# Performance work log

Measured on AMD Instinct MI355X. Metric: run time of the kernel, lower is better.

The kernel has to match this reference:

```python
import jax, jax.numpy as jnp
import numpy as np

DEPTH, DIM, HEADS, DH = 2, 1024, 16, 64
B, N, MEM, TEXT = 8, 256, 4, 64
PH, PW, PS = 4, 4, 16
EXP_H, EXP_W, EXP_T = 4, 4, 2
RH, RW, RT = 2*EXP_H+1, 2*EXP_W+1, 2*EXP_T+1  # 9,9,5
CUR_IDX = 20
MEM_IDXS = [0, 5, 10, 15]
SCALE = DH ** -0.5


def _pos(idx):
    # get_pos_from_idx_down_right
    nf = PH * PW
    inner = idx % nf
    return inner % PH, inner // PH, idx // nf


def _axial_freqs():
    # 2D axial rotary freqs over the (PH*PS)x(PW*PS) pixel grid, rot_dim = DH
    GH, GW = PH * PS, PW * PS
    nfa = DH // 4  # 16 base freqs per axis -> 32 dims per axis after pair-repeat
    inv = 1.0 / (10000.0 ** (np.arange(nfa, dtype=np.float64) / nfa))
    fh = np.repeat(np.arange(GH)[:, None] * inv[None, :], 2, axis=-1)  # [GH,32]
    fw = np.repeat(np.arange(GW)[:, None] * inv[None, :], 2, axis=-1)  # [GW,32]
    return np.concatenate([
        np.broadcast_to(fh[:, None, :], (GH, GW, DH // 2)),
        np.broadcast_to(fw[None, :, :], (GH, GW, DH // 2)),
    ], axis=-1).astype(np.float32)  # [GH,GW,DH]


def setup_inputs() -> dict:
    key = jax.random.key(0)
    ks = jax.random.split(key, 14)
    p = lambda k, shape: jax.random.normal(k, shape, jnp.float32) * 0.02
    x = jax.random.normal(ks[0], (B, N, DIM), jnp.float32)
    cond = jax.random.normal(ks[1], (B, MEM * N + TEXT, DIM), jnp.float32)
    Wq = p(ks[2], (DEPTH, DIM, HEADS * DH))
    Wk = p(ks[3], (DEPTH, DIM, HEADS * DH))
    Wv = p(ks[4], (DEPTH, DIM, HEADS * DH))
    Wo = p(ks[5], (DEPTH, HEADS * DH, DIM))
    bo = jnp.zeros((DEPTH, DIM), jnp.float32)
    rpe = p(ks[6], (DEPTH, RH * RW * RT, HEADS))
    W1 = p(ks[7], (DEPTH, DIM, DIM * 4 * 2))
    b1 = jnp.zeros((DEPTH, DIM * 8), jnp.float32)
    W2 = p(ks[8], (DEPTH, DIM * 4, DIM))
    b2 = jnp.zeros((DEPTH, DIM), jnp.float32)
    freqs = _axial_freqs()
    def block(idx):
        r, c, _ = _pos(idx)
        return freqs[r * PS:(r + 1) * PS, c * PS:(c + 1) * PS].reshape(-1, DH)
    src_freq = jnp.asarray(block(CUR_IDX))
    tgt_freq = jnp.asarray(np.concatenate([block(i) for i in MEM_IDXS], axis=0))
    sr, sc, st = _pos(CUR_IDX)
    rel = [(tr - sr + EXP_H) * RW + (tc - sc + EXP_W) + (tt - st + EXP_T) * RH * RW
           for (tr, tc, tt) in map(_pos, MEM_IDXS)]
    rel_idx = jnp.asarray(rel, jnp.int32)
    return dict(x=x, cond=cond, Wq=Wq, Wk=Wk, Wv=Wv, Wo=Wo, bo=bo, rpe=rpe,
                W1=W1, b1=b1, W2=W2, b2=b2, src_freq=src_freq, tgt_freq=tgt_freq,
                rel_idx=rel_idx)


def _rotate_half(t):
    # pairs interleaved: (d r) with r=2
    tr = t.reshape(t.shape[:-1] + (-1, 2))
    t1, t2 = tr[..., 0], tr[..., 1]
    return jnp.stack((-t2, t1), axis=-1).reshape(t.shape)


def _apply_rotary(freqs, t):
    return t * jnp.cos(freqs) + _rotate_half(t) * jnp.sin(freqs)


def reference(x, cond, Wq, Wk, Wv, Wo, bo, rpe, W1, b1, W2, b2, src_freq, tgt_freq, rel_idx):
    MS = MEM * N  # memory token count in cond
    split_heads = lambda t: t.reshape(t.shape[0], t.shape[1], HEADS, DH).transpose(0, 2, 1, 3)
    for l in range(DEPTH):
        # --- FullCrossAttention ---
        q = split_heads(x @ Wq[l])          # [b,h,n,dh]
        k = split_heads(cond @ Wk[l])       # [b,h,j,dh]
        v = split_heads(cond @ Wv[l])
        # gathered relative-position bias added to k (broadcast over feature dim)
        bias = rpe[l][rel_idx]              # [mem, h]
        bias_k = jnp.repeat(bias.T, N, axis=1)[None, :, :, None]  # [1,h,mem*S,1]
        k = k.at[:, :, :MS, :].add(bias_k)
        # inline rotary: src freqs on q, gathered target freqs on memory keys
        q = _apply_rotary(src_freq, q)
        k = k.at[:, :, :MS, :].set(_apply_rotary(tgt_freq, k[:, :, :MS, :]))
        dots = jnp.einsum('bhid,bhjd->bhij', q, k) * SCALE
        attn = jax.nn.softmax(dots, axis=-1)
        out = jnp.einsum('bhij,bhjd->bhid', attn, v)
        out = out.transpose(0, 2, 1, 3).reshape(x.shape[0], N, HEADS * DH)
        x = x + out @ Wo[l] + bo[l]
        # --- GEGLU FeedForward ---
        hgl = x @ W1[l] + b1[l]
        a, g = jnp.split(hgl, 2, axis=-1)
        y = a * jax.nn.gelu(g, approximate=False)
        x = x + y @ W2[l] + b2[l]
    return x
```

## Files before the change

kernel.cpp:

```cpp
#include <hip/hip_runtime.h>
#include <hip/hip_bf16.h>
#include <math.h>

typedef __hip_bfloat16 bf16;
typedef __bf16 bf16x8 __attribute__((ext_vector_type(8)));
typedef float f32x4 __attribute__((ext_vector_type(4)));

typedef __attribute__((address_space(3))) void lds_void;
typedef const __attribute__((address_space(1))) void gbl_void;

__device__ __forceinline__ float b2f(bf16 v) { return __bfloat162float(v); }
__device__ __forceinline__ bf16 f2b(float v) { return __float2bfloat16(v); }

__device__ __forceinline__ f32x4 shfl_xor4(f32x4 v, int m) {
  f32x4 o;
  o[0] = __shfl_xor(v[0], m);
  o[1] = __shfl_xor(v[1], m);
  o[2] = __shfl_xor(v[2], m);
  o[3] = __shfl_xor(v[3], m);
  return o;
}
__device__ __forceinline__ f32x4 max4(f32x4 a, f32x4 b) {
  f32x4 o;
  o[0] = fmaxf(a[0], b[0]); o[1] = fmaxf(a[1], b[1]);
  o[2] = fmaxf(a[2], b[2]); o[3] = fmaxf(a[3], b[3]);
  return o;
}
__device__ __forceinline__ f32x4 exp4(f32x4 a) {
  f32x4 o;
  o[0] = __expf(a[0]); o[1] = __expf(a[1]);
  o[2] = __expf(a[2]); o[3] = __expf(a[3]);
  return o;
}

__device__ __forceinline__ void cbar(int ahead) {
  if (ahead >= 2)      asm volatile("s_waitcnt vmcnt(8)" ::: "memory");
  else if (ahead == 1) asm volatile("s_waitcnt vmcnt(4)" ::: "memory");
  else                 asm volatile("s_waitcnt vmcnt(0)" ::: "memory");
  __builtin_amdgcn_s_barrier();
  __builtin_amdgcn_sched_barrier(0);
}

__global__ void detect_dtype(const unsigned int* __restrict__ x, int* __restrict__ flag) {
  int cnt = 0;
  for (int i = 0; i < 128; ++i) {
    unsigned int lo = x[i] & 0xFFFFu;
    unsigned int e = (lo >> 7) & 0xFFu;
    if (e >= 100u && e <= 140u) ++cnt;
  }
  *flag = (cnt >= 96) ? 1 : 0;
}

__global__ void convert_in(const void* __restrict__ src, bf16* __restrict__ dst,
                           int n, const int* __restrict__ flag) {
  int i = blockIdx.x * 256 + threadIdx.x;
  if (i >= n) return;
  dst[i] = (*flag) ? ((const bf16*)src)[i] : f2b(((const float*)src)[i]);
}

__global__ void emit_kernel(const float* __restrict__ xf, const int* __restrict__ flag,
                            void* __restrict__ out) {
  int i = blockIdx.x * 256 + threadIdx.x;
  if (*flag) ((bf16*)out)[i] = f2b(xf[i]);
  else       ((float*)out)[i] = xf[i];
}

template<int HALF>
__device__ __forceinline__ bf16x8 frag_ld(const __bf16* lt, int r, int quad) {
  constexpr int LB = (HALF == 128) ? 7 : 6;
  int line = r & (HALF - 1);
  int sl = (((r >> LB) << 2) | quad) ^ (line & 7);
  return *(const bf16x8*)&lt[line * 64 + sl * 8];
}

template<int TAG>
__global__ __launch_bounds__(256, 2) void gemm_bt(
    const bf16* __restrict__ A, int lda,
    const bf16* __restrict__ Bt, int ldb,
    float alpha,
    const float* __restrict__ resid,
    const bf16* __restrict__ bias,
    float* __restrict__ outf,
    bf16* __restrict__ outb,
    int ldc, int K)
{
  __shared__ char smem[65536] __attribute__((aligned(16)));
  float* lC = (float*)smem;

  int tid = threadIdx.x;
  int lane = tid & 63;
  int wave = tid >> 6;
  int quad = lane >> 4, l16 = lane & 15;
  int wm = (wave >> 1) * 64, wn = (wave & 1) * 64;
  int row0 = blockIdx.y * 128, col0 = blockIdx.x * 128;

  const bf16* asrc[2]; const bf16* bsrc[2];
#pragma unroll
  for (int i = 0; i < 2; ++i) {
    int line = i * 32 + (tid >> 3);
    int hx = (tid & 7) ^ (line & 7);
    int r = line + ((hx >> 2) << 6);
    int ke = (hx & 3) << 3;
    asrc[i] = A + (long long)(row0 + r) * lda + ke;
    bsrc[i] = Bt + (long long)(col0 + r) * ldb + ke;
  }

  auto stage = [&](int b, int t) {
    int o = t * 32;
#pragma unroll
    for (int i = 0; i < 2; ++i) {
      __builtin_amdgcn_global_load_lds((gbl_void*)(asrc[i] + o),
          (lds_void*)(smem + b * 8192 + i * 4096 + wave * 1024), 16, 0, 0);
      __builtin_amdgcn_global_load_lds((gbl_void*)(bsrc[i] + o),
          (lds_void*)(smem + 32768 + b * 8192 + i * 4096 + wave * 1024), 16, 0, 0);
    }
  };

  f32x4 acc[4][4];
#pragma unroll
  for (int a = 0; a < 4; ++a)
#pragma unroll
    for (int b = 0; b < 4; ++b) acc[a][b] = (f32x4){0.f, 0.f, 0.f, 0.f};

  int nk = K >> 5;
  stage(0, 0); stage(1, 1); stage(2, 2);
  cbar(2);

  for (int t = 0; t < nk; ++t) {
    if (t + 3 < nk) stage((t + 3) & 3, t + 3);
    const __bf16* lA = (const __bf16*)(smem + (t & 3) * 8192);
    const __bf16* lB = (const __bf16*)(smem + 32768 + (t & 3) * 8192);
    bf16x8 af[4], bfr[4];
#pragma unroll
    for (int mi = 0; mi < 4; ++mi) af[mi] = frag_ld<64>(lA, wm + mi * 16 + l16, quad);
#pragma unroll
    for (int ni = 0; ni < 4; ++ni) bfr[ni] = frag_ld<64>(lB, wn + ni * 16 + l16, quad);
    __builtin_amdgcn_s_setprio(1);
#pragma unroll
    for (int mi = 0; mi < 4; ++mi)
#pragma unroll
      for (int ni = 0; ni < 4; ++ni)
        acc[mi][ni] = __builtin_amdgcn_mfma_f32_16x16x32_bf16(
            af[mi], bfr[ni], acc[mi][ni], 0, 0, 0);
    __builtin_amdgcn_s_setprio(0);
    int hi = t + 3; if (hi > nk - 1) hi = nk - 1;
    cbar(hi - (t + 1));
  }

#pragma unroll
  for (int half = 0; half < 2; ++half) {
    __syncthreads();
    if ((wave >> 1) == half) {
#pragma unroll
      for (int mi = 0; mi < 4; ++mi)
#pragma unroll
        for (int ni = 0; ni < 4; ++ni)
#pragma unroll
          for (int r = 0; r < 4; ++r)
            lC[(mi * 16 + quad * 4 + r) * 128 + wn + ni * 16 + l16] =
                acc[mi][ni][r] * alpha;
    }
    __syncthreads();
#pragma unroll
    for (int i = 0; i < 8; ++i) {
      int f = i * 256 + tid;
      int row = f >> 5, cc = (f & 31) * 4;
      int m = row0 + half * 64 + row, n = col0 + cc;
      f32x4 v = *(const f32x4*)&lC[row * 128 + cc];
      long long ci = (long long)m * ldc + n;
      if (bias) {
        v[0] += b2f(bias[n]);     v[1] += b2f(bias[n + 1]);
        v[2] += b2f(bias[n + 2]); v[3] += b2f(bias[n + 3]);
      }
      if (resid) v += *(const f32x4*)&resid[ci];
      if (outf) *(f32x4*)&outf[ci] = v;
      if (outb) {
        bf16 c0 = f2b(v[0]), c1 = f2b(v[1]), c2 = f2b(v[2]), c3 = f2b(v[3]);
        ushort4 o = { *(unsigned short*)&c0, *(unsigned short*)&c1,
                      *(unsigned short*)&c2, *(unsigned short*)&c3 };
        *(ushort4*)&outb[ci] = o;
      }
    }
  }
}

__global__ __launch_bounds__(512, 2) void gemm256(
    const bf16* __restrict__ A, int lda,
    const bf16* __restrict__ Bt, int ldb,
    const bf16* __restrict__ bias,
    bf16* __restrict__ outb,
    int ldc, int K)
{
  __shared__ char smem[131072] __attribute__((aligned(16)));
  float* lC = (float*)smem;

  int tid = threadIdx.x;
  int lane = tid & 63;
  int wave = tid >> 6;
  int quad = lane >> 4, l16 = lane & 15;
  int wr = wave >> 2, wc = wave & 3;
  int wm = wr * 128, wn = wc * 64;
  int row0 = blockIdx.y * 256, col0 = blockIdx.x * 256;

  const bf16* asrc[2]; const bf16* bsrc[2];
#pragma unroll
  for (int i = 0; i < 2; ++i) {
    int line = i * 64 + (tid >> 3);
    int hx = (tid & 7) ^ (line & 7);
    int r = line + ((hx >> 2) << 7);
    int ke = (hx & 3) << 3;
    asrc[i] = A + (long long)(row0 + r) * lda + ke;
    bsrc[i] = Bt + (long long)(col0 + r) * ldb + ke;
  }

  auto stage = [&](int b, int t) {
    int o = t * 32;
#pragma unroll
    for (int i = 0; i < 2; ++i) {
      __builtin_amdgcn_global_load_lds((gbl_void*)(asrc[i] + o),
          (lds_void*)(smem + b * 16384 + i * 8192 + wave * 1024), 16, 0, 0);
      __builtin_amdgcn_global_load_lds((gbl_void*)(bsrc[i] + o),
          (lds_void*)(smem + 65536 + b * 16384 + i * 8192 + wave * 1024), 16, 0, 0);
    }
  };

  f32x4 acc[8][4];
#pragma unroll
  for (int a = 0; a < 8; ++a)
#pragma unroll
    for (int b = 0; b < 4; ++b) acc[a][b] = (f32x4){0.f, 0.f, 0.f, 0.f};

  int nk = K >> 5;
  stage(0, 0); stage(1, 1); stage(2, 2);
  cbar(2);

  for (int t = 0; t < nk; ++t) {
    if (t + 3 < nk) stage((t + 3) & 3, t + 3);
    const __bf16* lA = (const __bf16*)(smem + (t & 3) * 16384);
    const __bf16* lB = (const __bf16*)(smem + 65536 + (t & 3) * 16384);
    bf16x8 af[8], bfr[4];
#pragma unroll
    for (int mi = 0; mi < 8; ++mi) af[mi] = frag_ld<128>(lA, wm + mi * 16 + l16, quad);
#pragma unroll
    for (int ni = 0; ni < 4; ++ni) bfr[ni] = frag_ld<128>(lB, wn + ni * 16 + l16, quad);
    __builtin_amdgcn_s_setprio(1);
#pragma unroll
    for (int mi = 0; mi < 8; ++mi)
#pragma unroll
      for (int ni = 0; ni < 4; ++ni)
        acc[mi][ni] = __builtin_amdgcn_mfma_f32_16x16x32_bf16(
            af[mi], bfr[ni], acc[mi][ni], 0, 0, 0);
    __builtin_amdgcn_s_setprio(0);
    int hi = t + 3; if (hi > nk - 1) hi = nk - 1;
    cbar(hi - (t + 1));
  }

#pragma unroll
  for (int h = 0; h < 2; ++h) {
    __syncthreads();
    if (wr == h) {
#pragma unroll
      for (int mi = 0; mi < 8; ++mi)
#pragma unroll
        for (int ni = 0; ni < 4; ++ni)
#pragma unroll
          for (int r = 0; r < 4; ++r)
            lC[(mi * 16 + quad * 4 + r) * 256 + wn + ni * 16 + l16] =
                acc[mi][ni][r];
    }
    __syncthreads();
#pragma unroll
    for (int it = 0; it < 16; ++it) {
      int f = it * 512 + tid;
      int row = f >> 6, cc = (f & 63) * 4;
      int m = row0 + h * 128 + row, n = col0 + cc;
      f32x4 v = *(const f32x4*)&lC[row * 256 + cc];
      v[0] += b2f(bias[n]);     v[1] += b2f(bias[n + 1]);
      v[2] += b2f(bias[n + 2]); v[3] += b2f(bias[n + 3]);
      bf16 c0 = f2b(v[0]), c1 = f2b(v[1]), c2 = f2b(v[2]), c3 = f2b(v[3]);
      ushort4 o = { *(unsigned short*)&c0, *(unsigned short*)&c1,
                    *(unsigned short*)&c2, *(unsigned short*)&c3 };
      *(ushort4*)&outb[(long long)m * ldc + n] = o;
    }
  }
}

__global__ __launch_bounds__(256, 2) void gemm_splitk(
    const bf16* __restrict__ A, int lda,
    const bf16* __restrict__ Bt, int ldb,
    float* __restrict__ pbuf, int ldc, int M, int KC)
{
  __shared__ char smem[65536] __attribute__((aligned(16)));

  int koff = blockIdx.z * KC;
  float* outz = pbuf + (long long)blockIdx.z * M * ldc;
  int tid = threadIdx.x;
  int lane = tid & 63;
  int wave = tid >> 6;
  int quad = lane >> 4, l16 = lane & 15;
  int wm = (wave >> 1) * 64, wn = (wave & 1) * 64;
  int row0 = blockIdx.y * 128, col0 = blockIdx.x * 128;

  const bf16* asrc[2]; const bf16* bsrc[2];
#pragma unroll
  for (int i = 0; i < 2; ++i) {
    int line = i * 32 + (tid >> 3);
    int hx = (tid & 7) ^ (line & 7);
    int r = line + ((hx >> 2) << 6);
    int ke = (hx & 3) << 3;
    asrc[i] = A + (long long)(row0 + r) * lda + koff + ke;
    bsrc[i] = Bt + (long long)(col0 + r) * ldb + koff + ke;
  }

  auto stage = [&](int b, int t) {
    int o = t * 32;
#pragma unroll
    for (int i = 0; i < 2; ++i) {
      __builtin_amdgcn_global_load_lds((gbl_void*)(asrc[i] + o),
          (lds_void*)(smem + b * 8192 + i * 4096 + wave * 1024), 16, 0, 0);
      __builtin_amdgcn_global_load_lds((gbl_void*)(bsrc[i] + o),
          (lds_void*)(smem + 32768 + b * 8192 + i * 4096 + wave * 1024), 16, 0, 0);
    }
  };

  f32x4 acc[4][4];
#pragma unroll
  for (int a = 0; a < 4; ++a)
#pragma unroll
    for (int b = 0; b < 4; ++b) acc[a][b] = (f32x4){0.f, 0.f, 0.f, 0.f};

  int nk = KC >> 5;
  stage(0, 0); stage(1, 1); stage(2, 2);
  cbar(2);

  for (int t = 0; t < nk; ++t) {
    if (t + 3 < nk) stage((t + 3) & 3, t + 3);
    const __bf16* lA = (const __bf16*)(smem + (t & 3) * 8192);
    const __bf16* lB = (const __bf16*)(smem + 32768 + (t & 3) * 8192);
    bf16x8 af[4], bfr[4];
#pragma unroll
    for (int mi = 0; mi < 4; ++mi) af[mi] = frag_ld<64>(lA, wm + mi * 16 + l16, quad);
#pragma unroll
    for (int ni = 0; ni < 4; ++ni) bfr[ni] = frag_ld<64>(lB, wn + ni * 16 + l16, quad);
    __builtin_amdgcn_s_setprio(1);
#pragma unroll
    for (int mi = 0; mi < 4; ++mi)
#pragma unroll
      for (int ni = 0; ni < 4; ++ni)
        acc[mi][ni] = __builtin_amdgcn_mfma_f32_16x16x32_bf16(
            af[mi], bfr[ni], acc[mi][ni], 0, 0, 0);
    __builtin_amdgcn_s_setprio(0);
    int hi = t + 3; if (hi > nk - 1) hi = nk - 1;
    cbar(hi - (t + 1));
  }

#pragma unroll
  for (int mi = 0; mi < 4; ++mi)
#pragma unroll
    for (int ni = 0; ni < 4; ++ni) {
      int n = col0 + wn + ni * 16 + l16;
#pragma unroll
      for (int r = 0; r < 4; ++r) {
        int m = row0 + wm + mi * 16 + quad * 4 + r;
        outz[(long long)m * ldc + n] = acc[mi][ni][r];
      }
    }
}

__global__ void reduce_ff2(const float* __restrict__ pbuf, const bf16* __restrict__ bias,
                           float* __restrict__ xf, bf16* __restrict__ xbf) {
  int i = blockIdx.x * 256 + threadIdx.x;
  const int NT = 2048 * 1024;
  float v = xf[i] + b2f(bias[i & 1023]) +
            pbuf[i] + pbuf[i + NT] + pbuf[i + 2 * NT] + pbuf[i + 3 * NT];
  xf[i] = v;
  xbf[i] = f2b(v);
}

__device__ __forceinline__ void fa_stage(
    const bf16* __restrict__ kb, const bf16* __restrict__ vtb, int j0, int tk,
    char* smem, int kboff, int vboff, int tid, int wave)
{
  int rounds = tk >> 6;
  for (int i = 0; i < rounds; ++i) {
    int rowk = i * 64 + (tid >> 3);
    int cbk = ((tid & 7) * 16) ^ ((rowk & 7) << 4);
    __builtin_amdgcn_global_load_lds(
        (gbl_void*)(kb + (long long)(j0 + rowk) * 1024 + (cbk >> 1)),
        (lds_void*)(smem + kboff + i * 8192 + wave * 1024), 16, 0, 0);
    int rowv, cbv;
    if (tk == 128) { rowv = i * 32 + (tid >> 4); cbv = ((tid & 15) * 16) ^ ((rowv & 7) << 4); }
    else           { rowv = (tid >> 3);          cbv = ((tid & 7) * 16) ^ ((rowv & 7) << 4); }
    __builtin_amdgcn_global_load_lds(
        (gbl_void*)(vtb + (long long)rowv * 8704 + j0 + (cbv >> 1)),
        (lds_void*)(smem + vboff + i * 8192 + wave * 1024), 16, 0, 0);
  }
}

template<int TK>
__device__ __forceinline__ void fa_compute(
    const char* smem, int kboff, int vboff,
    const bf16x8 (&qa)[2], bf16* lPw,
    int quad, int l16,
    f32x4 (&accO)[4], f32x4& mrow, f32x4& lrow)
{
  constexpr int NT = TK / 16;
  constexpr int NCH = TK / 32;
  const __bf16* lK = (const __bf16*)(smem + kboff);
  const __bf16* lV = (const __bf16*)(smem + vboff);
  int xork = (l16 & 7) << 3;

  f32x4 accS[NT];
#pragma unroll
  for (int ni = 0; ni < NT; ++ni) accS[ni] = (f32x4){0.f, 0.f, 0.f, 0.f};

#pragma unroll
  for (int ni = 0; ni < NT; ++ni)
#pragma unroll
    for (int ks = 0; ks < 2; ++ks) {
      bf16x8 bfr = *(const bf16x8*)&lK[(ni * 16 + l16) * 64 + ((ks * 32 + quad * 8) ^ xork)];
      accS[ni] = __builtin_amdgcn_mfma_f32_16x16x32_bf16(qa[ks], bfr, accS[ni], 0, 0, 0);
    }

  f32x4 vmax = (f32x4){-INFINITY, -INFINITY, -INFINITY, -INFINITY};
#pragma unroll
  for (int ni = 0; ni < NT; ++ni) {
    accS[ni] *= 0.125f;
    vmax = max4(vmax, accS[ni]);
  }
#pragma unroll
  for (int m = 1; m <= 8; m <<= 1) vmax = max4(vmax, shfl_xor4(vmax, m));
  f32x4 mnew = max4(mrow, vmax);
  f32x4 alpha = exp4(mrow - mnew);
  f32x4 rs = (f32x4){0.f, 0.f, 0.f, 0.f};
#pragma unroll
  for (int ni = 0; ni < NT; ++ni) {
    accS[ni] = exp4(accS[ni] - mnew);
    rs += accS[ni];
  }
#pragma unroll
  for (int m = 1; m <= 8; m <<= 1) rs += shfl_xor4(rs, m);
  lrow = lrow * alpha + rs;
  mrow = mnew;
#pragma unroll
  for (int nd = 0; nd < 4; ++nd) accO[nd] *= alpha;

#pragma unroll
  for (int c = 0; c < NCH; ++c) {
#pragma unroll
    for (int u = 0; u < 2; ++u)
#pragma unroll
      for (int r = 0; r < 4; ++r)
        lPw[(quad * 4 + r) * 40 + u * 16 + l16] = f2b(accS[c * 2 + u][r]);
    bf16x8 pa = *(const bf16x8*)&lPw[l16 * 40 + quad * 8];
#pragma unroll
    for (int nd = 0; nd < 4; ++nd) {
      bf16x8 vb = *(const bf16x8*)&lV[(nd * 16 + l16) * TK + ((c * 32 + quad * 8) ^ xork)];
      accO[nd] = __builtin_amdgcn_mfma_f32_16x16x32_bf16(pa, vb, accO[nd], 0, 0, 0);
    }
  }
}

__global__ __launch_bounds__(512, 2) void flash_attn(
    const bf16* __restrict__ q, const bf16* __restrict__ k,
    const bf16* __restrict__ vt, bf16* __restrict__ att)
{
  __shared__ char smem[75776] __attribute__((aligned(16)));

  int idx = blockIdx.x;
  int b = idx >> 5, h = (idx >> 1) & 15, half = idx & 1;
  int tid = threadIdx.x, wave = tid >> 6, lane = tid & 63;
  int quad = lane >> 4, l16 = lane & 15;
  int qrow0 = b * 256 + half * 128 + wave * 16;

  const bf16* kb  = k  + (long long)b * 1088 * 1024 + h * 64;
  const bf16* vtb = vt + (long long)(h * 64) * 8704 + b * 1088;
  bf16* lPw = (bf16*)(smem + 65536 + wave * 1280);

  bf16x8 qa[2];
#pragma unroll
  for (int ks = 0; ks < 2; ++ks)
    qa[ks] = *(const bf16x8*)&q[(long long)(qrow0 + l16) * 1024 +
                                h * 64 + ks * 32 + quad * 8];

  f32x4 accO[4];
  f32x4 mrow = (f32x4){-INFINITY, -INFINITY, -INFINITY, -INFINITY};
  f32x4 lrow = (f32x4){0.f, 0.f, 0.f, 0.f};
#pragma unroll
  for (int nd = 0; nd < 4; ++nd) accO[nd] = (f32x4){0.f, 0.f, 0.f, 0.f};

  fa_stage(kb, vtb, 0, 128, smem, 0, 32768, tid, wave);
  __syncthreads();

  for (int jt = 0; jt < 8; ++jt) {
    int buf = (jt & 1) * 16384;
    int nbuf = 16384 - buf;
    if (jt < 7) fa_stage(kb, vtb, (jt + 1) * 128, 128, smem, nbuf, 32768 + nbuf, tid, wave);
    else        fa_stage(kb, vtb, 1024, 64, smem, nbuf, 32768 + nbuf, tid, wave);
    fa_compute<128>(smem, buf, 32768 + buf, qa, lPw, quad, l16, accO, mrow, lrow);
    __syncthreads();
  }
  fa_compute<64>(smem, 0, 32768, qa, lPw, quad, l16, accO, mrow, lrow);

  f32x4 inv;
  inv[0] = 1.f / lrow[0]; inv[1] = 1.f / lrow[1];
  inv[2] = 1.f / lrow[2]; inv[3] = 1.f / lrow[3];
#pragma unroll
  for (int nd = 0; nd < 4; ++nd) {
    f32x4 o = accO[nd] * inv;
#pragma unroll
    for (int r = 0; r < 4; ++r)
      att[(long long)(qrow0 + quad * 4 + r) * 1024 +
          h * 64 + nd * 16 + l16] = f2b(o[r]);
  }
}

__global__ void init_x_kernel(const void* __restrict__ x, const int* __restrict__ flag,
                              float* __restrict__ xf, bf16* __restrict__ xbf) {
  int i = blockIdx.x * 256 + threadIdx.x;
  float v = (*flag) ? b2f(((const bf16*)x)[i]) : ((const float*)x)[i];
  xf[i] = v;
  xbf[i] = f2b(v);
}

__global__ void transpose_w(const void* __restrict__ in, bf16* __restrict__ out,
                            int R, int C, const int* __restrict__ flag) {
  __shared__ bf16 tile[32][33];
  long long zoff = (long long)blockIdx.z * R * C;
  const bf16* inb = (const bf16*)in + zoff;
  const float* inf = (const float*)in + zoff;
  out += zoff;
  int tx = threadIdx.x, ty = threadIdx.y;
  int c0 = blockIdx.x * 32, r0 = blockIdx.y * 32;
  int isb = *flag;
#pragma unroll
  for (int i = 0; i < 4; ++i) {
    long long off = (long long)(r0 + ty + i * 8) * C + (c0 + tx);
    tile[ty + i * 8][tx] = isb ? inb[off] : f2b(inf[off]);
  }
  __syncthreads();
#pragma unroll
  for (int i = 0; i < 4; ++i)
    out[(long long)(c0 + ty + i * 8) * R + (r0 + tx)] = tile[tx][ty + i * 8];
}

__global__ void rotary_q_kernel(bf16* __restrict__ q, const bf16* __restrict__ srcf) {
  int idx = blockIdx.x * 256 + threadIdx.x;
  int row = idx >> 9;
  int p = idx & 511;
  int h = p >> 5, i = p & 31;
  int d0 = h * 64 + 2 * i;
  int ntok = row & 255;
  float f = b2f(srcf[ntok * 64 + 2 * i]);
  float c = cosf(f), s = sinf(f);
  long long base = (long long)row * 1024 + d0;
  float q0 = b2f(q[base]), q1 = b2f(q[base + 1]);
  q[base]     = f2b(q0 * c - q1 * s);
  q[base + 1] = f2b(q1 * c + q0 * s);
}

__global__ void k_bias_rot_kernel(bf16* __restrict__ k, const bf16* __restrict__ tgtf,
                                  const bf16* __restrict__ rpe,
                                  const int* __restrict__ ridx, int layer) {
  int idx = blockIdx.x * 256 + threadIdx.x;
  int b = idx >> 19;
  int rem = idx & ((1 << 19) - 1);
  int j = rem >> 9;
  int p = rem & 511;
  int h = p >> 5, i = p & 31;
  int d0 = h * 64 + 2 * i;
  float bias = b2f(rpe[(layer * 405 + ridx[j >> 8]) * 16 + h]);
  float f = b2f(tgtf[j * 64 + 2 * i]);
  float c = cosf(f), s = sinf(f);
  long long base = (long long)(b * 1088 + j) * 1024 + d0;
  float k0 = b2f(k[base]) + bias, k1 = b2f(k[base + 1]) + bias;
  k[base]     = f2b(k0 * c - k1 * s);
  k[base + 1] = f2b(k1 * c + k0 * s);
}

__global__ void geglu_kernel(const bf16* __restrict__ hgl, bf16* __restrict__ y) {
  int idx = blockIdx.x * 256 + threadIdx.x;
  int m = idx >> 12, n = idx & 4095;
  float a = b2f(hgl[(long long)m * 8192 + n]);
  float g = b2f(hgl[(long long)m * 8192 + 4096 + n]);
  float ge = 0.5f * g * (1.0f + erff(g * 0.70710678118654752f));
  y[idx] = f2b(a * ge);
}

extern "C" void kernel_launch(void* const* d_in, const int* in_sizes, int n_in,
                              void* d_out, int out_size, void* d_ws, size_t ws_size,
                              hipStream_t stream) {
  (void)in_sizes; (void)n_in; (void)out_size; (void)ws_size;
  const void* x    = d_in[0];
  const void* cond = d_in[1];
  const void* Wq   = d_in[2];
  const void* Wk   = d_in[3];
  const void* Wv   = d_in[4];
  const void* Wo   = d_in[5];
  const void* bo   = d_in[6];
  const void* rpe  = d_in[7];
  const void* W1   = d_in[8];
  const void* b1   = d_in[9];
  const void* W2   = d_in[10];
  const void* b2   = d_in[11];
  const void* srcf = d_in[12];
  const void* tgtf = d_in[13];
  const int*  ridx = (const int*)d_in[14];

  char* w = (char*)d_ws;
  int* flag = (int*)w;   w += 256;
  bf16* WqT = (bf16*)w;  w += (size_t)2 * 1024 * 1024 * 2;
  bf16* WkT = (bf16*)w;  w += (size_t)2 * 1024 * 1024 * 2;
  bf16* WvT = (bf16*)w;  w += (size_t)2 * 1024 * 1024 * 2;
  bf16* WoT = (bf16*)w;  w += (size_t)2 * 1024 * 1024 * 2;
  bf16* W1T = (bf16*)w;  w += (size_t)2 * 8192 * 1024 * 2;
  bf16* W2T = (bf16*)w;  w += (size_t)2 * 4096 * 1024 * 2;
  bf16* condb = (bf16*)w; w += (size_t)8704 * 1024 * 2;
  bf16* bo_b = (bf16*)w;  w += 2048 * 2;
  bf16* rpe_b = (bf16*)w; w += 12960 * 2;
  bf16* b1_b = (bf16*)w;  w += 16384 * 2;
  bf16* b2_b = (bf16*)w;  w += 2048 * 2;
  bf16* srcf_b = (bf16*)w; w += 16384 * 2;
  bf16* tgtf_b = (bf16*)w; w += 65536 * 2;
  float* xf = (float*)w; w += (size_t)2048 * 1024 * 4;
  bf16* xbf = (bf16*)w;  w += (size_t)2048 * 1024 * 2;
  bf16* qbuf = (bf16*)w; w += (size_t)2048 * 1024 * 2;
  bf16* kbuf = (bf16*)w; w += (size_t)8704 * 1024 * 2;
  bf16* vTf = (bf16*)w;  w += (size_t)1024 * 8704 * 2;
  bf16* att = (bf16*)w;  w += (size_t)2048 * 1024 * 2;
  bf16* hgl = (bf16*)w;  w += (size_t)2048 * 8192 * 2;
  bf16* ybuf = (bf16*)w; w += (size_t)2048 * 4096 * 2;
  float* pbuf = (float*)hgl;

  detect_dtype<<<1, 1, 0, stream>>>((const unsigned int*)x, flag);

  convert_in<<<34816, 256, 0, stream>>>(cond, condb, 8704 * 1024, flag);
  convert_in<<<8, 256, 0, stream>>>(bo, bo_b, 2048, flag);
  convert_in<<<51, 256, 0, stream>>>(rpe, rpe_b, 12960, flag);
  convert_in<<<64, 256, 0, stream>>>(b1, b1_b, 16384, flag);
  convert_in<<<8, 256, 0, stream>>>(b2, b2_b, 2048, flag);
  convert_in<<<64, 256, 0, stream>>>(srcf, srcf_b, 16384, flag);
  convert_in<<<256, 256, 0, stream>>>(tgtf, tgtf_b, 65536, flag);

  dim3 tb(32, 8);
  transpose_w<<<dim3(32, 32, 2),  tb, 0, stream>>>(Wq, WqT, 1024, 1024, flag);
  transpose_w<<<dim3(32, 32, 2),  tb, 0, stream>>>(Wk, WkT, 1024, 1024, flag);
  transpose_w<<<dim3(32, 32, 2),  tb, 0, stream>>>(Wv, WvT, 1024, 1024, flag);
  transpose_w<<<dim3(32, 32, 2),  tb, 0, stream>>>(Wo, WoT, 1024, 1024, flag);
  transpose_w<<<dim3(256, 32, 2), tb, 0, stream>>>(W1, W1T, 1024, 8192, flag);
  transpose_w<<<dim3(32, 128, 2), tb, 0, stream>>>(W2, W2T, 4096, 1024, flag);
  init_x_kernel<<<8192, 256, 0, stream>>>(x, flag, xf, xbf);

  for (int l = 0; l < 2; ++l) {
    const bf16* WqTl = WqT + (size_t)l * 1024 * 1024;
    const bf16* WkTl = WkT + (size_t)l * 1024 * 1024;
    const bf16* WvTl = WvT + (size_t)l * 1024 * 1024;
    const bf16* WoTl = WoT + (size_t)l * 1024 * 1024;
    const bf16* W1Tl = W1T + (size_t)l * 8192 * 1024;
    const bf16* W2Tl = W2T + (size_t)l * 4096 * 1024;

    gemm_bt<0><<<dim3(8, 16), 256, 0, stream>>>(xbf, 1024, WqTl, 1024, 1.f,
        nullptr, nullptr, nullptr, qbuf, 1024, 1024);
    rotary_q_kernel<<<4096, 256, 0, stream>>>(qbuf, srcf_b);
    gemm_bt<1><<<dim3(68, 8), 256, 0, stream>>>(WvTl, 1024, condb, 1024, 1.f,
        nullptr, nullptr, nullptr, vTf, 8704, 1024);
    gemm_bt<2><<<dim3(8, 68), 256, 0, stream>>>(condb, 1024, WkTl, 1024, 1.f,
        nullptr, nullptr, nullptr, kbuf, 1024, 1024);
    k_bias_rot_kernel<<<16384, 256, 0, stream>>>(kbuf, tgtf_b, rpe_b, ridx, l);
    flash_attn<<<256, 512, 0, stream>>>(qbuf, kbuf, vTf, att);
    gemm_bt<3><<<dim3(8, 16), 256, 0, stream>>>(att, 1024, WoTl, 1024, 1.f,
        xf, bo_b + (size_t)l * 1024, xf, xbf, 1024, 1024);
    gemm256<<<dim3(32, 8), 512, 0, stream>>>(xbf, 1024, W1Tl, 1024,
        b1_b + (size_t)l * 8192, hgl, 8192, 1024);
    geglu_kernel<<<32768, 256, 0, stream>>>(hgl, ybuf);
    gemm_splitk<<<dim3(8, 16, 4), 256, 0, stream>>>(ybuf, 4096, W2Tl, 4096,
                                                    pbuf, 1024, 2048, 1024);
    reduce_ff2<<<8192, 256, 0, stream>>>(pbuf, b2_b + (size_t)l * 1024, xf, xbf);
  }

  emit_kernel<<<8192, 256, 0, stream>>>(xf, flag, d_out);
}
```

Baseline: 783.9 us.

## Fuse GEGLU into FF1 GEMM, add XCD swizzle, use triple-buffered GEMM

The FF1 GEMM now loads the matching value and gate columns of W1 into the same tile and applies the bias and exact GELU gating in its epilogue. This removes the separate geglu kernel and the round trip of the 8192-wide hidden tensor through memory. The 128x128 GEMMs drop from a 4-stage to a 3-stage LDS pipeline, cutting shared memory from 64KB to 48KB so three blocks can fit per CU. Workgroup IDs in the GEMMs and flash attention are also remapped so neighbouring tiles land on the same XCD for L2 reuse. The shallower prefetch trades some latency hiding for the higher occupancy.

```diff
diff --git a/kernel.cpp b/kernel.cpp
--- a/kernel.cpp
+++ b/kernel.cpp
@@ -40,6 +40,18 @@
   __builtin_amdgcn_s_barrier();
   __builtin_amdgcn_sched_barrier(0);
 }
+__device__ __forceinline__ void cbar2(int ahead) {
+  if (ahead >= 1) asm volatile("s_waitcnt vmcnt(4)" ::: "memory");
+  else            asm volatile("s_waitcnt vmcnt(0)" ::: "memory");
+  __builtin_amdgcn_s_barrier();
+  __builtin_amdgcn_sched_barrier(0);
+}
+
+__device__ __forceinline__ int xcd_swz(int flat, int nwg) {
+  int q = nwg >> 3, r = nwg & 7;
+  int xcd = flat & 7, pos = flat >> 3;
+  return (xcd < r) ? (xcd * (q + 1) + pos) : (r * (q + 1) + (xcd - r) * q + pos);
+}
 
 __global__ void detect_dtype(const unsigned int* __restrict__ x, int* __restrict__ flag) {
   int cnt = 0;
@@ -74,7 +86,7 @@
 }
 
 template<int TAG>
-__global__ __launch_bounds__(256, 2) void gemm_bt(
+__global__ __launch_bounds__(256, 3) void gemm_bt(
     const bf16* __restrict__ A, int lda,
     const bf16* __restrict__ Bt, int ldb,
     float alpha,
@@ -84,7 +96,7 @@
     bf16* __restrict__ outb,
     int ldc, int K)
 {
-  __shared__ char smem[65536] __attribute__((aligned(16)));
+  __shared__ char smem[49152] __attribute__((aligned(16)));
   float* lC = (float*)smem;
 
   int tid = threadIdx.x;
@@ -92,7 +104,17 @@
   int wave = tid >> 6;
   int quad = lane >> 4, l16 = lane & 15;
   int wm = (wave >> 1) * 64, wn = (wave & 1) * 64;
-  int row0 = blockIdx.y * 128, col0 = blockIdx.x * 128;
+
+  int gx = gridDim.x, gy = gridDim.y;
+  int nwg = gx * gy;
+  bool ymaj = gy >= gx;
+  int flat = ymaj ? ((int)blockIdx.y * gx + blockIdx.x)
+                  : ((int)blockIdx.x * gy + blockIdx.y);
+  int swz = xcd_swz(flat, nwg);
+  int bx, by;
+  if (ymaj) { by = swz / gx; bx = swz - by * gx; }
+  else      { bx = swz / gy; by = swz - bx * gy; }
+  int row0 = by * 128, col0 = bx * 128;
 
   const bf16* asrc[2]; const bf16* bsrc[2];
 #pragma unroll
@@ -112,7 +134,7 @@
       __builtin_amdgcn_global_load_lds((gbl_void*)(asrc[i] + o),
           (lds_void*)(smem + b * 8192 + i * 4096 + wave * 1024), 16, 0, 0);
       __builtin_amdgcn_global_load_lds((gbl_void*)(bsrc[i] + o),
-          (lds_void*)(smem + 32768 + b * 8192 + i * 4096 + wave * 1024), 16, 0, 0);
+          (lds_void*)(smem + 24576 + b * 8192 + i * 4096 + wave * 1024), 16, 0, 0);
     }
   };
 
@@ -123,13 +145,14 @@
     for (int b = 0; b < 4; ++b) acc[a][b] = (f32x4){0.f, 0.f, 0.f, 0.f};
 
   int nk = K >> 5;
-  stage(0, 0); stage(1, 1); stage(2, 2);
-  cbar(2);
+  stage(0, 0); stage(1, 1);
+  cbar2(1);
 
   for (int t = 0; t < nk; ++t) {
-    if (t + 3 < nk) stage((t + 3) & 3, t + 3);
-    const __bf16* lA = (const __bf16*)(smem + (t & 3) * 8192);
-    const __bf16* lB = (const __bf16*)(smem + 32768 + (t & 3) * 8192);
+    if (t + 2 < nk) stage((t + 2) % 3, t + 2);
+    int bt = t % 3;
+    const __bf16* lA = (const __bf16*)(smem + bt * 8192);
+    const __bf16* lB = (const __bf16*)(smem + 24576 + bt * 8192);
     bf16x8 af[4], bfr[4];
 #pragma unroll
     for (int mi = 0; mi < 4; ++mi) af[mi] = frag_ld<64>(lA, wm + mi * 16 + l16, quad);
@@ -143,8 +166,8 @@
         acc[mi][ni] = __builtin_amdgcn_mfma_f32_16x16x32_bf16(
             af[mi], bfr[ni], acc[mi][ni], 0, 0, 0);
     __builtin_amdgcn_s_setprio(0);
-    int hi = t + 3; if (hi > nk - 1) hi = nk - 1;
-    cbar(hi - (t + 1));
+    int ahead = nk - 1 - (t + 1); if (ahead > 1) ahead = 1;
+    cbar2(ahead);
   }
 
 #pragma unroll
@@ -184,12 +207,11 @@
   }
 }
 
-__global__ __launch_bounds__(512, 2) void gemm256(
+__global__ __launch_bounds__(512, 2) void gemm256_geglu(
     const bf16* __restrict__ A, int lda,
-    const bf16* __restrict__ Bt, int ldb,
+    const bf16* __restrict__ W1t, int ldb,
     const bf16* __restrict__ bias,
-    bf16* __restrict__ outb,
-    int ldc, int K)
+    bf16* __restrict__ outy, int ldy, int K)
 {
   __shared__ char smem[131072] __attribute__((aligned(16)));
   float* lC = (float*)smem;
@@ -200,17 +222,18 @@
   int quad = lane >> 4, l16 = lane & 15;
   int wr = wave >> 2, wc = wave & 3;
   int wm = wr * 128, wn = wc * 64;
-  int row0 = blockIdx.y * 256, col0 = blockIdx.x * 256;
+  int row0 = blockIdx.y * 256, col0 = blockIdx.x * 128;
 
   const bf16* asrc[2]; const bf16* bsrc[2];
 #pragma unroll
   for (int i = 0; i < 2; ++i) {
     int line = i * 64 + (tid >> 3);
     int hx = (tid & 7) ^ (line & 7);
-    int r = line + ((hx >> 2) << 7);
+    int rA = line + ((hx >> 2) << 7);
     int ke = (hx & 3) << 3;
-    asrc[i] = A + (long long)(row0 + r) * lda + ke;
-    bsrc[i] = Bt + (long long)(col0 + r) * ldb + ke;
+    asrc[i] = A + (long long)(row0 + rA) * lda + ke;
+    int rowW = (hx & 4) ? (4096 + col0 + line) : (col0 + line);
+    bsrc[i] = W1t + (long long)rowW * ldb + ke;
   }
 
   auto stage = [&](int b, int t) {
@@ -270,27 +293,33 @@
     }
     __syncthreads();
 #pragma unroll
-    for (int it = 0; it < 16; ++it) {
+    for (int it = 0; it < 8; ++it) {
       int f = it * 512 + tid;
-      int row = f >> 6, cc = (f & 63) * 4;
+      int row = f >> 5, cc = (f & 31) * 4;
       int m = row0 + h * 128 + row, n = col0 + cc;
-      f32x4 v = *(const f32x4*)&lC[row * 256 + cc];
-      v[0] += b2f(bias[n]);     v[1] += b2f(bias[n + 1]);
-      v[2] += b2f(bias[n + 2]); v[3] += b2f(bias[n + 3]);
-      bf16 c0 = f2b(v[0]), c1 = f2b(v[1]), c2 = f2b(v[2]), c3 = f2b(v[3]);
-      ushort4 o = { *(unsigned short*)&c0, *(unsigned short*)&c1,
-                    *(unsigned short*)&c2, *(unsigned short*)&c3 };
-      *(ushort4*)&outb[(long long)m * ldc + n] = o;
-    }
-  }
-}
-
-__global__ __launch_bounds__(256, 2) void gemm_splitk(
+      f32x4 a = *(const f32x4*)&lC[row * 256 + cc];
+      f32x4 g = *(const f32x4*)&lC[row * 256 + 128 + cc];
+      bf16 yb[4];
+#pragma unroll
+      for (int j = 0; j < 4; ++j) {
+        float av = a[j] + b2f(bias[n + j]);
+        float gv = g[j] + b2f(bias[4096 + n + j]);
+        float ge = 0.5f * gv * (1.0f + erff(gv * 0.70710678118654752f));
+        yb[j] = f2b(av * ge);
+      }
+      ushort4 o = { *(unsigned short*)&yb[0], *(unsigned short*)&yb[1],
+                    *(unsigned short*)&yb[2], *(unsigned short*)&yb[3] };
+      *(ushort4*)&outy[(long long)m * ldy + n] = o;
+    }
+  }
+}
+
+__global__ __launch_bounds__(256, 3) void gemm_splitk(
     const bf16* __restrict__ A, int lda,
     const bf16* __restrict__ Bt, int ldb,
     float* __restrict__ pbuf, int ldc, int M, int KC)
 {
-  __shared__ char smem[65536] __attribute__((aligned(16)));
+  __shared__ char smem[49152] __attribute__((aligned(16)));
 
   int koff = blockIdx.z * KC;
   float* outz = pbuf + (long long)blockIdx.z * M * ldc;
@@ -299,7 +328,17 @@
   int wave = tid >> 6;
   int quad = lane >> 4, l16 = lane & 15;
   int wm = (wave >> 1) * 64, wn = (wave & 1) * 64;
-  int row0 = blockIdx.y * 128, col0 = blockIdx.x * 128;
+
+  int gx = gridDim.x, gy = gridDim.y;
+  int nwg = gx * gy;
+  bool ymaj = gy >= gx;
+  int flat = ymaj ? ((int)blockIdx.y * gx + blockIdx.x)
+                  : ((int)blockIdx.x * gy + blockIdx.y);
+  int swz = xcd_swz(flat, nwg);
+  int bx, by;
+  if (ymaj) { by = swz / gx; bx = swz - by * gx; }
+  else      { bx = swz / gy; by = swz - bx * gy; }
+  int row0 = by * 128, col0 = bx * 128;
 
   const bf16* asrc[2]; const bf16* bsrc[2];
 #pragma unroll
@@ -319,7 +358,7 @@
       __builtin_amdgcn_global_load_lds((gbl_void*)(asrc[i] + o),
           (lds_void*)(smem + b * 8192 + i * 4096 + wave * 1024), 16, 0, 0);
       __builtin_amdgcn_global_load_lds((gbl_void*)(bsrc[i] + o),
-          (lds_void*)(smem + 32768 + b * 8192 + i * 4096 + wave * 1024), 16, 0, 0);
+          (lds_void*)(smem + 24576 + b * 8192 + i * 4096 + wave * 1024), 16, 0, 0);
     }
   };
 
@@ -330,13 +369,14 @@
     for (int b = 0; b < 4; ++b) acc[a][b] = (f32x4){0.f, 0.f, 0.f, 0.f};
 
   int nk = KC >> 5;
-  stage(0, 0); stage(1, 1); stage(2, 2);
-  cbar(2);
+  stage(0, 0); stage(1, 1);
+  cbar2(1);
 
   for (int t = 0; t < nk; ++t) {
-    if (t + 3 < nk) stage((t + 3) & 3, t + 3);
-    const __bf16* lA = (const __bf16*)(smem + (t & 3) * 8192);
-    const __bf16* lB = (const __bf16*)(smem + 32768 + (t & 3) * 8192);
+    if (t + 2 < nk) stage((t + 2) % 3, t + 2);
+    int bt = t % 3;
+    const __bf16* lA = (const __bf16*)(smem + bt * 8192);
+    const __bf16* lB = (const __bf16*)(smem + 24576 + bt * 8192);
     bf16x8 af[4], bfr[4];
 #pragma unroll
     for (int mi = 0; mi < 4; ++mi) af[mi] = frag_ld<64>(lA, wm + mi * 16 + l16, quad);
@@ -350,8 +390,8 @@
         acc[mi][ni] = __builtin_amdgcn_mfma_f32_16x16x32_bf16(
             af[mi], bfr[ni], acc[mi][ni], 0, 0, 0);
     __builtin_amdgcn_s_setprio(0);
-    int hi = t + 3; if (hi > nk - 1) hi = nk - 1;
-    cbar(hi - (t + 1));
+    int ahead = nk - 1 - (t + 1); if (ahead > 1) ahead = 1;
+    cbar2(ahead);
   }
 
 #pragma unroll
@@ -467,7 +507,7 @@
 {
   __shared__ char smem[75776] __attribute__((aligned(16)));
 
-  int idx = blockIdx.x;
+  int idx = xcd_swz(blockIdx.x, gridDim.x);
   int b = idx >> 5, h = (idx >> 1) & 15, half = idx & 1;
   int tid = threadIdx.x, wave = tid >> 6, lane = tid & 63;
   int quad = lane >> 4, l16 = lane & 15;
@@ -576,15 +616,6 @@
   float k0 = b2f(k[base]) + bias, k1 = b2f(k[base + 1]) + bias;
   k[base]     = f2b(k0 * c - k1 * s);
   k[base + 1] = f2b(k1 * c + k0 * s);
-}
-
-__global__ void geglu_kernel(const bf16* __restrict__ hgl, bf16* __restrict__ y) {
-  int idx = blockIdx.x * 256 + threadIdx.x;
-  int m = idx >> 12, n = idx & 4095;
-  float a = b2f(hgl[(long long)m * 8192 + n]);
-  float g = b2f(hgl[(long long)m * 8192 + 4096 + n]);
-  float ge = 0.5f * g * (1.0f + erff(g * 0.70710678118654752f));
-  y[idx] = f2b(a * ge);
 }
 
 extern "C" void kernel_launch(void* const* d_in, const int* in_sizes, int n_in,
@@ -670,9 +701,8 @@
     flash_attn<<<256, 512, 0, stream>>>(qbuf, kbuf, vTf, att);
     gemm_bt<3><<<dim3(8, 16), 256, 0, stream>>>(att, 1024, WoTl, 1024, 1.f,
         xf, bo_b + (size_t)l * 1024, xf, xbf, 1024, 1024);
-    gemm256<<<dim3(32, 8), 512, 0, stream>>>(xbf, 1024, W1Tl, 1024,
-        b1_b + (size_t)l * 8192, hgl, 8192, 1024);
-    geglu_kernel<<<32768, 256, 0, stream>>>(hgl, ybuf);
+    gemm256_geglu<<<dim3(32, 8), 512, 0, stream>>>(xbf, 1024, W1Tl, 1024,
+        b1_b + (size_t)l * 8192, ybuf, 4096, 1024);
     gemm_splitk<<<dim3(8, 16, 4), 256, 0, stream>>>(ybuf, 4096, W2Tl, 4096,
                                                     pbuf, 1024, 2048, 1024);
     reduce_ff2<<<8192, 256, 0, stream>>>(pbuf, b2_b + (size_t)l * 1024, xf, xbf);
```

Result: faster. 743.0 us (-5.2%).
